# Kernel optimization log

Measured on AMD Instinct MI355X. Metric: run time of the kernel, lower is better.

Reference implementation:

```python
import jax, jax.numpy as jnp
import numpy as np

N = 50000       # nodes
E = 1600000     # edges (before self-loops)
DIN = 128       # input_dim
HID = 32        # hidden_dim per head
H = 4           # num_heads
HD = HID * H    # 128, concat-head width
DOUT = 128      # output_dim
NC = 2          # num_classes
G = 256         # graphs in batch
NEG_SLOPE = 0.2
BN_EPS = 1e-5


def setup_inputs() -> dict:
    key = jax.random.key(0)
    ks = jax.random.split(key, 20)
    p = lambda k, shp: (jax.random.normal(k, shp, jnp.float32) * 0.05)
    x = jax.random.normal(ks[0], (N, DIN), jnp.float32)
    edge_index = jax.random.randint(ks[1], (2, E), 0, N, dtype=jnp.int32)
    batch = jnp.sort(jax.random.randint(ks[2], (N,), 0, G, dtype=jnp.int32))
    return {
        "x": x, "edge_index": edge_index, "batch": batch,
        # GATConv 1: lin weight [DIN, H*HID], att vectors [H, HID], bias [H*HID]
        "W1": p(ks[3], (DIN, HD)), "a1_src": p(ks[4], (H, HID)), "a1_dst": p(ks[5], (H, HID)), "b1": p(ks[6], (HD,)),
        "bn1_g": jnp.ones((HD,), jnp.float32), "bn1_b": jnp.zeros((HD,), jnp.float32),
        # GATConv 2: in = H*HID
        "W2": p(ks[7], (HD, HD)), "a2_src": p(ks[8], (H, HID)), "a2_dst": p(ks[9], (H, HID)), "b2": p(ks[10], (HD,)),
        "bn2_g": jnp.ones((HD,), jnp.float32), "bn2_b": jnp.zeros((HD,), jnp.float32),
        "L1W": p(ks[11], (HD, DOUT)), "L1b": p(ks[12], (DOUT,)),
        "L2W": p(ks[13], (DOUT, NC)), "L2b": p(ks[14], (NC,)),
    }


def _add_self_loops(edge_index, n):
    loops = jnp.arange(n, dtype=edge_index.dtype)
    return jnp.concatenate([edge_index, jnp.stack([loops, loops])], axis=1)


def _gat_conv(x, edge_index, W, a_src, a_dst, bias):
    # PyG GATConv: h = x @ W -> [N,H,F]; per-edge score = LeakyReLU(a_src.h_src + a_dst.h_dst);
    # softmax over incoming edges of each dst node; weighted scatter-add; concat heads + bias.
    n = x.shape[0]
    h = (x @ W).reshape(n, H, HID)
    src, dst = edge_index[0], edge_index[1]
    alpha_s = jnp.sum(h * a_src[None], axis=-1)   # [N,H]
    alpha_d = jnp.sum(h * a_dst[None], axis=-1)   # [N,H]
    e = jax.nn.leaky_relu(alpha_s[src] + alpha_d[dst], NEG_SLOPE)  # [E,H]
    m = jax.ops.segment_max(e, dst, num_segments=n)                # stable softmax over neighbors
    ex = jnp.exp(e - m[dst])
    s = jax.ops.segment_sum(ex, dst, num_segments=n)
    alpha = ex / (s[dst] + 1e-16)                                  # [E,H]
    out = jax.ops.segment_sum(h[src] * alpha[:, :, None], dst, num_segments=n)  # [N,H,F]
    return out.reshape(n, H * HID) + bias


def _batch_norm(x, gamma, beta):
    mu = jnp.mean(x, axis=0)
    var = jnp.mean((x - mu) ** 2, axis=0)
    return gamma * (x - mu) * jax.lax.rsqrt(var + BN_EPS) + beta


def reference(x, edge_index, batch, W1, a1_src, a1_dst, b1, bn1_g, bn1_b,
              W2, a2_src, a2_dst, b2, bn2_g, bn2_b, L1W, L1b, L2W, L2b):
    ei = _add_self_loops(edge_index, x.shape[0])
    h = jax.nn.relu(_gat_conv(x, ei, W1, a1_src, a1_dst, b1))
    h = _batch_norm(h, bn1_g, bn1_b)
    h = jax.nn.relu(_gat_conv(h, ei, W2, a2_src, a2_dst, b2))
    h = _batch_norm(h, bn2_g, bn2_b)
    # global mean pool over graph ids
    sums = jax.ops.segment_sum(h, batch, num_segments=G)
    cnts = jax.ops.segment_sum(jnp.ones((h.shape[0],), h.dtype), batch, num_segments=G)
    pooled = sums / jnp.maximum(cnts, 1.0)[:, None]   # [G, HD]
    z = jax.nn.relu(pooled @ L1W + L1b)               # dropout inactive at eval
    return z @ L2W + L2b                              # [G, NC]
```

## Files before the change

### kernel.cpp

```cpp
#include <hip/hip_runtime.h>
#include <math.h>

#define NN 50000
#define EE 1600000
#define GG 256
#define PAD 80
#define NB 256
#define EPB 6250
#define NR 8
#define RNG 6250
#define BCAP 960
#define BNPB 512
#define BNPR 98

constexpr float NEG = 0.2f;
constexpr float BN_EPS = 1e-5f;

typedef __attribute__((ext_vector_type(8))) short short8;
typedef __attribute__((ext_vector_type(4))) float f32x4;
typedef __attribute__((ext_vector_type(2))) float f32x2;

constexpr int PB_W1 = 0, PB_A1S = 16384, PB_A1D = 16512, PB_B1 = 16640,
              PB_G1 = 16768, PB_BE1 = 16896, PB_W2 = 17024, PB_A2S = 33408,
              PB_A2D = 33536, PB_B2 = 33664, PB_G2 = 33792, PB_BE2 = 33920,
              PB_L1W = 34048, PB_L1B = 50432, PB_L2W = 50560, PB_L2B = 50816,
              PB_TOTAL = 50818;

struct PtrPack { const void* p[16]; };

__device__ __forceinline__ float b2f(unsigned short u) {
  unsigned v = ((unsigned)u) << 16;
  float f;
  __builtin_memcpy(&f, &v, 4);
  return f;
}
__device__ __forceinline__ float b2f_lo(unsigned u) {
  unsigned v = u << 16;
  float f;
  __builtin_memcpy(&f, &v, 4);
  return f;
}
__device__ __forceinline__ float b2f_hi(unsigned u) {
  unsigned v = u & 0xffff0000u;
  float f;
  __builtin_memcpy(&f, &v, 4);
  return f;
}
__device__ __forceinline__ unsigned short f2b(float f) {
  unsigned x;
  __builtin_memcpy(&x, &f, 4);
  unsigned r = x + 0x7FFFu + ((x >> 16) & 1u);
  return (unsigned short)(r >> 16);
}

__device__ __forceinline__ void pkfma(f32x2& acc, unsigned u, f32x2 wp) {
  f32x2 p = {b2f_lo(u), b2f_hi(u)};
  asm("v_pk_fma_f32 %0, %1, %2, %0" : "+v"(acc) : "v"(p), "v"(wp));
}

__global__ __launch_bounds__(512) void k_prep(PtrPack pk, const unsigned short* __restrict__ xb,
                                              const int* __restrict__ batch,
                                              const int* __restrict__ esrc,
                                              const int* __restrict__ edst,
                                              int* __restrict__ flag,
                                              float* __restrict__ pb,
                                              int* __restrict__ starts, float* __restrict__ bnacc,
                                              int* __restrict__ ctrs,
                                              unsigned char* __restrict__ hist,
                                              unsigned* __restrict__ buck, int* __restrict__ bcnt,
                                              unsigned short* __restrict__ Wt1,
                                              float* __restrict__ wzero,
                                              float* __restrict__ poolsum) {
  const int segoff[17] = {0, 16384, 16512, 16640, 16768, 16896, 17024, 33408,
                          33536, 33664, 33792, 33920, 34048, 50432, 50560, 50816, 50818};
  __shared__ unsigned hcnt[25000];
  __shared__ int bc[NR];
  __shared__ int cs;
  int c = blockIdx.x, t = threadIdx.x;
  if (t == 0) cs = 0;
  if (t < NR) bc[t] = 0;
  for (int j = t; j < 25000; j += 512) hcnt[j] = 0u;
  __syncthreads();
  int sane = 0;
  for (int i = t; i < 4096; i += 512) {
    float a = fabsf(b2f(xb[i]));
    if (a > 1e-4f && a < 100.f) sane++;
  }
  atomicAdd(&cs, sane);
  int e0 = c * EPB;
  for (int i = t; i < EPB; i += 512) {
    int e = e0 + i;
    int d = edst[e];
    if ((unsigned)d >= (unsigned)NN) continue;
    int s = esrc[e];
    if ((unsigned)s >= (unsigned)NN) s = 0;
    int sh = (d & 1) * 16;
    unsigned old = atomicAdd(&hcnt[d >> 1], 1u << sh);
    unsigned rank = (old >> sh) & 0xFFFFu;
    if (rank > 7u) continue;
    int r = d / RNG;
    int dl = d - r * RNG;
    int pos = atomicAdd(&bc[r], 1);
    if (pos < BCAP)
      buck[(c * NR + r) * BCAP + pos] = ((unsigned)s << 16) | ((unsigned)dl << 3) | rank;
  }
  __syncthreads();
  int bf = (cs > 3482) ? 1 : 0;
  if (c == 0 && t == 0) *flag = bf;
  if (t < NR) bcnt[c * NR + t] = min(bc[t], BCAP);
  unsigned* hw = (unsigned*)(hist + c * NN);
  for (int j = t; j < NN / 4; j += 512) {
    unsigned w0 = hcnt[2 * j], w1 = hcnt[2 * j + 1];
    unsigned b0 = min(w0 & 0xFFFFu, 255u), b1 = min(w0 >> 16, 255u);
    unsigned b2 = min(w1 & 0xFFFFu, 255u), b3 = min(w1 >> 16, 255u);
    hw[j] = b0 | (b1 << 8) | (b2 << 16) | (b3 << 24);
  }
  for (int j = t; j < 199; j += 512) {
    int i = c * 199 + j;
    if (i < PB_TOTAL) {
      int seg = 0;
      while (i >= segoff[seg + 1]) seg++;
      int k = i - segoff[seg];
      pb[i] = bf ? b2f(((const unsigned short*)pk.p[seg])[k]) : ((const float*)pk.p[seg])[k];
    }
  }
  for (int j = t; j < 64; j += 512) {
    int i = c * 64 + j;
    int n = i & 127, k = i >> 7;
    Wt1[n * 128 + k] = bf ? ((const unsigned short*)pk.p[0])[k * 128 + n]
                          : f2b(((const float*)pk.p[0])[k * 128 + n]);
  }
  for (int j = t; j < 128; j += 512) poolsum[c * 128 + j] = 0.f;
  if (t < 32) bnacc[c * 32 + t] = 0.f;
  for (int j = t; j < 196; j += 512) {
    int n = c * 196 + j;
    if (n < NN) {
      int bb = batch[n];
      bb = min(max(bb, 0), GG - 1);
      int bp = (n == 0) ? -1 : batch[n - 1];
      bp = min(max(bp, -1), GG - 1);
      for (int gg = bp + 1; gg <= bb; gg++) starts[gg] = n;
      if (n == NN - 1)
        for (int gg = bb + 1; gg <= GG; gg++) starts[gg] = NN;
    }
  }
  if (c == 255 && t < 8) ctrs[t] = 0;
}

__device__ __forceinline__ void gemm_body(float* cst, int bid,
                                          const unsigned short* __restrict__ Xb,
                                          const float* __restrict__ Xf, int bfm,
                                          const unsigned short* __restrict__ Wt,
                                          const float* __restrict__ shiftW,
                                          const float* __restrict__ aS,
                                          const float* __restrict__ aD,
                                          unsigned short* __restrict__ Y,
                                          float* __restrict__ as_, float* __restrict__ ad_) {
  int t = threadIdx.x;
  int row0 = bid * 64;
  int w = t >> 6, lane = t & 63;
  int m = lane & 15, quad = lane >> 4;
  int rA = min(row0 + w * 16 + m, NN - 1);
  short8 a4[4];
  if (bfm) {
    const short8* xp = (const short8*)(Xb + rA * 128);
#pragma unroll
    for (int kk = 0; kk < 4; kk++) a4[kk] = xp[kk * 4 + quad];
  } else {
#pragma unroll
    for (int kk = 0; kk < 4; kk++) {
      const float* xf = Xf + rA * 128 + kk * 32 + quad * 8;
#pragma unroll
      for (int j = 0; j < 8; j++) a4[kk][j] = (short)f2b(xf[j]);
    }
  }
  f32x4 acc[8] = {};
#pragma unroll
  for (int kk = 0; kk < 4; kk++) {
    int ko = kk * 32 + quad * 8;
#pragma unroll
    for (int n0 = 0; n0 < 8; n0++) {
      short8 b = *(const short8*)(Wt + (n0 * 16 + m) * 128 + ko);
      acc[n0] = __builtin_amdgcn_mfma_f32_16x16x32_bf16(a4[kk], b, acc[n0], 0, 0, 0);
    }
  }
#pragma unroll
  for (int n0 = 0; n0 < 8; n0++)
#pragma unroll
    for (int r = 0; r < 4; r++)
      cst[(w * 16 + quad * 4 + r) * 130 + n0 * 16 + m] = acc[n0][r];
  __syncthreads();
  int cg = t & 31, rg = t >> 5;
  int c0 = cg * 4;
  float a_s[4], a_d[4], sw[4];
#pragma unroll
  for (int j = 0; j < 4; j++) {
    a_s[j] = aS[c0 + j];
    a_d[j] = aD[c0 + j];
    sw[j] = shiftW[c0 + j];
  }
#pragma unroll
  for (int i = 0; i < 8; i++) {
    int rl = rg + i * 8;
    int row = row0 + rl;
    float v0 = cst[rl * 130 + c0 + 0] + sw[0];
    float v1 = cst[rl * 130 + c0 + 1] + sw[1];
    float v2 = cst[rl * 130 + c0 + 2] + sw[2];
    float v3 = cst[rl * 130 + c0 + 3] + sw[3];
    if (row < NN) {
      uint2 pk2;
      pk2.x = (unsigned)f2b(v0) | ((unsigned)f2b(v1) << 16);
      pk2.y = (unsigned)f2b(v2) | ((unsigned)f2b(v3) << 16);
      *reinterpret_cast<uint2*>(&Y[row * 128 + c0]) = pk2;
    }
    float ps = v0 * a_s[0] + v1 * a_s[1] + v2 * a_s[2] + v3 * a_s[3];
    float pd = v0 * a_d[0] + v1 * a_d[1] + v2 * a_d[2] + v3 * a_d[3];
    ps += __shfl_xor(ps, 1); ps += __shfl_xor(ps, 2); ps += __shfl_xor(ps, 4);
    pd += __shfl_xor(pd, 1); pd += __shfl_xor(pd, 2); pd += __shfl_xor(pd, 4);
    if ((cg & 7) == 0 && row < NN) {
      int hh = cg >> 3;
      as_[row * 4 + hh] = ps;
      ad_[row * 4 + hh] = pd;
    }
  }
}

__global__ __launch_bounds__(256) void k_basegemm(unsigned char* __restrict__ hist,
                                                  int* __restrict__ cnt,
                                                  const unsigned short* __restrict__ Xb,
                                                  const float* __restrict__ Xf,
                                                  const int* __restrict__ flagp,
                                                  const unsigned short* __restrict__ Wt,
                                                  const float* __restrict__ shiftW,
                                                  const float* __restrict__ aS,
                                                  const float* __restrict__ aD,
                                                  unsigned short* __restrict__ Y,
                                                  float* __restrict__ as_, float* __restrict__ ad_) {
  __shared__ float cst[64 * 130];
  int idx = blockIdx.x;
  if (idx < 196) {
    int d = idx * 256 + threadIdx.x;
    if (d >= NN) return;
    int run = 0;
    for (int b = 0; b < NB; b += 16) {
      unsigned char h[16];
#pragma unroll
      for (int j = 0; j < 16; j++) h[j] = hist[(b + j) * NN + d];
#pragma unroll
      for (int j = 0; j < 16; j++) {
        hist[(b + j) * NN + d] = (unsigned char)min(run, 255);
        run += h[j];
      }
    }
    cnt[d] = run;
  } else {
    gemm_body(cst, idx - 196, Xb, Xf, *flagp, Wt, shiftW, aS, aD, Y, as_, ad_);
  }
}

__global__ __launch_bounds__(256) void k_fill(const unsigned* __restrict__ buck,
                                              const int* __restrict__ bcnt,
                                              const unsigned char* __restrict__ base,
                                              unsigned short* __restrict__ adj) {
  int idx = blockIdx.x;
  int t = threadIdx.x;
  int r = idx & 7, g = idx >> 3;
  int dbase = r * RNG;
#pragma unroll 1
  for (int j = 0; j < 8; j++) {
    int c = g * 8 + j;
    int n = bcnt[c * NR + r];
    const unsigned* bk = buck + (c * NR + r) * BCAP;
    const unsigned char* bs = base + c * NN;
    for (int i = t; i < n; i += 256) {
      unsigned p = bk[i];
      int s = p >> 16;
      int dl = (p >> 3) & 0x1FFF;
      int rank = p & 7;
      int d = dbase + dl;
      int slot = (int)bs[d] + rank;
      if (slot < PAD) adj[d * PAD + slot] = (unsigned short)s;
    }
  }
}

__global__ __launch_bounds__(256) void k_gemm(const unsigned short* __restrict__ Xb,
                                              const unsigned short* __restrict__ Wt,
                                              const float* __restrict__ shiftW,
                                              const float* __restrict__ aS,
                                              const float* __restrict__ aD,
                                              unsigned short* __restrict__ Y,
                                              float* __restrict__ as_, float* __restrict__ ad_) {
  __shared__ float cst[64 * 130];
  gemm_body(cst, blockIdx.x, Xb, nullptr, 1, Wt, shiftW, aS, aD, Y, as_, ad_);
}

__global__ __launch_bounds__(256) void k_agg(const unsigned short* __restrict__ adj,
                                             const int* __restrict__ cnt,
                                             const float4* __restrict__ asrc4,
                                             const float4* __restrict__ adst4,
                                             const uint4* __restrict__ hin4,
                                             const float* __restrict__ bias,
                                             unsigned short* __restrict__ out) {
  __shared__ float wq2[4][4][PAD];
  __shared__ unsigned soffs[4][PAD];
  int t = threadIdx.x;
  int wid = t >> 6, lane = t & 63;
  int n = blockIdx.x * 4 + wid;
  int deg = cnt[n];
  if (deg < 0) deg = 0;
  if (deg > PAD - 1) deg = PAD - 1;
  int tot = deg + 1;
  int W = (((tot + 3) >> 2) + 3) & ~3;
  int WL = 4 * W;
  int beg = n * PAD;
  float4 ad4 = adst4[n];
  float ls0 = 0.f, ls1 = 0.f, ls2 = 0.f, ls3 = 0.f;
  for (int b = lane; b < WL; b += 64) {
    if (b < tot) {
      int s = (b < deg) ? (int)adj[beg + b] : n;
      if ((unsigned)s >= (unsigned)NN) s = n;
      float4 a = asrc4[s];
      float s0 = a.x + ad4.x; s0 = s0 > 0.f ? s0 : NEG * s0;
      float s1 = a.y + ad4.y; s1 = s1 > 0.f ? s1 : NEG * s1;
      float s2 = a.z + ad4.z; s2 = s2 > 0.f ? s2 : NEG * s2;
      float s3 = a.w + ad4.w; s3 = s3 > 0.f ? s3 : NEG * s3;
      float e0 = __expf(s0), e1 = __expf(s1), e2 = __expf(s2), e3 = __expf(s3);
      ls0 += e0; ls1 += e1; ls2 += e2; ls3 += e3;
      wq2[wid][0][b] = e0; wq2[wid][1][b] = e1;
      wq2[wid][2][b] = e2; wq2[wid][3][b] = e3;
      soffs[wid][b] = (unsigned)s * 256u;
    } else {
      wq2[wid][0][b] = 0.f; wq2[wid][1][b] = 0.f;
      wq2[wid][2][b] = 0.f; wq2[wid][3][b] = 0.f;
      soffs[wid][b] = (unsigned)n * 256u;
    }
  }
  asm volatile("" ::: "memory");
  __builtin_amdgcn_wave_barrier();
  int g = lane >> 4, L = lane & 15, hd = L >> 2;
  const char* hb = (const char*)hin4;
  unsigned Loff = (unsigned)L * 16u;
  const float* wrow = &wq2[wid][hd][0];
  const unsigned* srow = &soffs[wid][0];
  f32x2 acc2[4] = {};
  int e0w = g * W, e1w = e0w + W;
  for (int e = e0w; e < e1w; e += 4) {
    f32x4 w4 = *(const f32x4*)(wrow + e);
    uint4 o4 = *(const uint4*)(srow + e);
    uint4 v1 = *(const uint4*)(hb + (o4.x + Loff));
    uint4 v2 = *(const uint4*)(hb + (o4.y + Loff));
    uint4 v3 = *(const uint4*)(hb + (o4.z + Loff));
    uint4 v4 = *(const uint4*)(hb + (o4.w + Loff));
    f32x2 p1 = {w4.x, w4.x}, p2 = {w4.y, w4.y}, p3 = {w4.z, w4.z}, p4 = {w4.w, w4.w};
    pkfma(acc2[0], v1.x, p1); pkfma(acc2[1], v1.y, p1);
    pkfma(acc2[2], v1.z, p1); pkfma(acc2[3], v1.w, p1);
    pkfma(acc2[0], v2.x, p2); pkfma(acc2[1], v2.y, p2);
    pkfma(acc2[2], v2.z, p2); pkfma(acc2[3], v2.w, p2);
    pkfma(acc2[0], v3.x, p3); pkfma(acc2[1], v3.y, p3);
    pkfma(acc2[2], v3.z, p3); pkfma(acc2[3], v3.w, p3);
    pkfma(acc2[0], v4.x, p4); pkfma(acc2[1], v4.y, p4);
    pkfma(acc2[2], v4.z, p4); pkfma(acc2[3], v4.w, p4);
  }
#pragma unroll
  for (int j = 0; j < 4; j++) {
    acc2[j].x += __shfl_xor(acc2[j].x, 16);
    acc2[j].y += __shfl_xor(acc2[j].y, 16);
    acc2[j].x += __shfl_xor(acc2[j].x, 32);
    acc2[j].y += __shfl_xor(acc2[j].y, 32);
  }
#pragma unroll
  for (int mm = 1; mm < 64; mm <<= 1) {
    ls0 += __shfl_xor(ls0, mm);
    ls1 += __shfl_xor(ls1, mm);
    ls2 += __shfl_xor(ls2, mm);
    ls3 += __shfl_xor(ls3, mm);
  }
  if (g == 0) {
    float den = (hd == 0) ? ls0 : (hd == 1) ? ls1 : (hd == 2) ? ls2 : ls3;
    float inv = 1.0f / (den + 1e-16f);
    const float4* bp = reinterpret_cast<const float4*>(bias + L * 8);
    float4 b0 = bp[0], b1 = bp[1];
    float o0 = acc2[0].x * inv + b0.x;
    float o1 = acc2[0].y * inv + b0.y;
    float o2 = acc2[1].x * inv + b0.z;
    float o3 = acc2[1].y * inv + b0.w;
    float o4 = acc2[2].x * inv + b1.x;
    float o5 = acc2[2].y * inv + b1.y;
    float o6 = acc2[3].x * inv + b1.z;
    float o7 = acc2[3].y * inv + b1.w;
    o0 = o0 > 0.f ? o0 : 0.f;
    o1 = o1 > 0.f ? o1 : 0.f;
    o2 = o2 > 0.f ? o2 : 0.f;
    o3 = o3 > 0.f ? o3 : 0.f;
    o4 = o4 > 0.f ? o4 : 0.f;
    o5 = o5 > 0.f ? o5 : 0.f;
    o6 = o6 > 0.f ? o6 : 0.f;
    o7 = o7 > 0.f ? o7 : 0.f;
    uint4 pk4;
    pk4.x = (unsigned)f2b(o0) | ((unsigned)f2b(o1) << 16);
    pk4.y = (unsigned)f2b(o2) | ((unsigned)f2b(o3) << 16);
    pk4.z = (unsigned)f2b(o4) | ((unsigned)f2b(o5) << 16);
    pk4.w = (unsigned)f2b(o6) | ((unsigned)f2b(o7) << 16);
    *reinterpret_cast<uint4*>(&out[n * 128 + L * 8]) = pk4;
  }
}

__global__ __launch_bounds__(256) void k_bnpartial(const unsigned* __restrict__ x32,
                                                   float* __restrict__ partial,
                                                   const int* __restrict__ starts,
                                                   float* __restrict__ poolsum) {
  __shared__ float stg[4][256];
  int bid = blockIdx.x, t = threadIdx.x;
  int u = t & 63, ph = t >> 6;
  if (bid < BNPB) {
    int r0 = bid * BNPR, r1 = min(r0 + BNPR, NN);
    float s0 = 0.f, q0 = 0.f, s1 = 0.f, q1 = 0.f;
    for (int r = r0 + ph; r < r1; r += 4) {
      unsigned v = x32[r * 64 + u];
      float lo = b2f_lo(v), hi = b2f_hi(v);
      s0 += lo; q0 += lo * lo;
      s1 += hi; q1 += hi * hi;
    }
    stg[ph][2 * u] = s0;
    stg[ph][2 * u + 1] = s1;
    stg[ph][128 + 2 * u] = q0;
    stg[ph][128 + 2 * u + 1] = q1;
    __syncthreads();
    partial[bid * 256 + t] = stg[0][t] + stg[1][t] + stg[2][t] + stg[3][t];
  } else {
    int g = bid - BNPB;
    int b0 = starts[g], b1 = starts[g + 1];
    b0 = min(max(b0, 0), NN);
    b1 = min(max(b1, 0), NN);
    float p0 = 0.f, p1 = 0.f;
    for (int r = b0 + ph; r < b1; r += 4) {
      unsigned v = x32[r * 64 + u];
      p0 += b2f_lo(v);
      p1 += b2f_hi(v);
    }
    stg[ph][2 * u] = p0;
    stg[ph][2 * u + 1] = p1;
    __syncthreads();
    if (t < 128) poolsum[g * 128 + t] = stg[0][t] + stg[1][t] + stg[2][t] + stg[3][t];
  }
}

__global__ __launch_bounds__(256) void k_bnfinal(const float* __restrict__ partial,
                                                 const float* __restrict__ g, const float* __restrict__ b,
                                                 float* __restrict__ scale, float* __restrict__ shift,
                                                 const float* __restrict__ W2f, float* __restrict__ sw2,
                                                 unsigned short* __restrict__ Wt2) {
  __shared__ float sums[256];
  __shared__ float shs[128];
  __shared__ float scs[128];
  int t = threadIdx.x;
  float acc = 0.f;
  for (int bb = 0; bb < BNPB; bb += 8) {
    float a0 = partial[(bb + 0) * 256 + t];
    float a1 = partial[(bb + 1) * 256 + t];
    float a2 = partial[(bb + 2) * 256 + t];
    float a3 = partial[(bb + 3) * 256 + t];
    float a4 = partial[(bb + 4) * 256 + t];
    float a5 = partial[(bb + 5) * 256 + t];
    float a6 = partial[(bb + 6) * 256 + t];
    float a7 = partial[(bb + 7) * 256 + t];
    acc += ((a0 + a1) + (a2 + a3)) + ((a4 + a5) + (a6 + a7));
  }
  sums[t] = acc;
  __syncthreads();
  if (t < 128) {
    float inv = 1.0f / NN;
    float mu = sums[t] * inv;
    float var = sums[128 + t] * inv - mu * mu;
    float rs = rsqrtf(var + BN_EPS);
    float sc = g[t] * rs;
    float shv = b[t] - mu * sc;
    scale[t] = sc;
    shift[t] = shv;
    shs[t] = shv;
    scs[t] = sc;
  }
  __syncthreads();
  if (W2f) {
    if (t < 128) {
      float s = 0.f;
      for (int k = 0; k < 128; k++) s += shs[k] * W2f[k * 128 + t];
      sw2[t] = s;
    }
    for (int i = t; i < 16384; i += 256) {
      int n = i & 127, k = i >> 7;
      Wt2[n * 128 + k] = f2b(scs[k] * W2f[k * 128 + n]);
    }
  }
}

__global__ __launch_bounds__(128) void k_head(const float* __restrict__ poolsum,
                                              const int* __restrict__ starts,
                                              const float* __restrict__ scale, const float* __restrict__ shift,
                                              const float* __restrict__ L1W, const float* __restrict__ L1b,
                                              const float* __restrict__ L2W, const float* __restrict__ L2b,
                                              const int* __restrict__ flagp, void* __restrict__ outp) {
  int g = blockIdx.x, t = threadIdx.x;
  int b0 = starts[g], b1 = starts[g + 1];
  b0 = min(max(b0, 0), NN);
  b1 = min(max(b1, 0), NN);
  int cnt = b1 - b0;
  __shared__ float pooled[128];
  float s = poolsum[g * 128 + t];
  pooled[t] = (cnt > 0) ? (s / cnt) * scale[t] + shift[t] : 0.f;
  __syncthreads();
  float z = L1b[t];
  for (int k = 0; k < 128; k++) z += pooled[k] * L1W[k * 128 + t];
  z = z > 0.f ? z : 0.f;
  __shared__ float r0a[128], r1a[128];
  r0a[t] = z * L2W[t * 2 + 0];
  r1a[t] = z * L2W[t * 2 + 1];
  __syncthreads();
  for (int d = 64; d >= 1; d >>= 1) {
    if (t < d) {
      r0a[t] += r0a[t + d];
      r1a[t] += r1a[t + d];
    }
    __syncthreads();
  }
  if (t == 0) {
    float o0 = r0a[0] + L2b[0];
    float o1 = r1a[0] + L2b[1];
    if (*flagp) {
      unsigned short* ob = (unsigned short*)outp;
      ob[g * 2 + 0] = f2b(o0);
      ob[g * 2 + 1] = f2b(o1);
    } else {
      float* of = (float*)outp;
      of[g * 2 + 0] = o0;
      of[g * 2 + 1] = o1;
    }
  }
}

extern "C" void kernel_launch(void* const* d_in, const int* in_sizes, int n_in,
                              void* d_out, int out_size, void* d_ws, size_t ws_size,
                              hipStream_t stream) {
  (void)in_sizes; (void)n_in; (void)out_size; (void)ws_size;
  const int* ei = (const int*)d_in[1];
  const int* batch = (const int*)d_in[2];

  float* ws = (float*)d_ws;
  size_t o = 0;
  int* flag = (int*)(ws + o);   o += 16;
  int* ctrs = (int*)(ws + o);   o += 16;
  float* pb = ws + o;           o += 51200;
  float* bnacc = ws + o;        o += 8192;
  float* bnpart = ws + o;       o += BNPB * 256;
  float* scale1 = ws + o;       o += 128;
  float* shift1 = ws + o;       o += 128;
  float* scale2 = ws + o;       o += 128;
  float* shift2 = ws + o;       o += 128;
  float* wzero = ws + o;        o += 128;
  float* sw2 = ws + o;          o += 128;
  unsigned short* Wt1 = (unsigned short*)(ws + o); o += 8192;
  unsigned short* Wt2 = (unsigned short*)(ws + o); o += 8192;
  float* poolsum = ws + o;      o += GG * 128;
  int* cnt = (int*)(ws + o);    o += 50016;
  int* starts = (int*)(ws + o); o += 512;
  int* bcnt = (int*)(ws + o);   o += 2048;
  float* asrc = ws + o;         o += 200000;
  float* adst = ws + o;         o += 200000;
  unsigned* buck = (unsigned*)(ws + o);            o += NB * NR * BCAP;
  unsigned short* adj = (unsigned short*)(ws + o); o += NN * PAD / 2;
  unsigned short* hA = (unsigned short*)(ws + o);  o += 3200000;
  unsigned short* hB = (unsigned short*)(ws + o);  o += 3200000;

  unsigned char* hist = (unsigned char*)hA;

  const int* esrc = ei;
  const int* edst = ei + EE;

  PtrPack pk;
  for (int i = 0; i < 16; i++) pk.p[i] = d_in[3 + i];

  k_prep<<<NB, 512, 0, stream>>>(pk, (const unsigned short*)d_in[0], batch, esrc, edst,
                                 flag, pb, starts, bnacc, ctrs, hist, buck, bcnt,
                                 Wt1, wzero, poolsum);

  k_basegemm<<<196 + 782, 256, 0, stream>>>(hist, cnt,
                                            (const unsigned short*)d_in[0], (const float*)d_in[0],
                                            flag, Wt1, wzero,
                                            pb + PB_A1S, pb + PB_A1D, hB, asrc, adst);
  k_fill<<<NB, 256, 0, stream>>>(buck, bcnt, hist, adj);
  k_agg<<<NN / 4, 256, 0, stream>>>(adj, cnt, (const float4*)asrc, (const float4*)adst,
                                    (const uint4*)hB, pb + PB_B1, hA);
  k_bnpartial<<<BNPB, 256, 0, stream>>>((const unsigned*)hA, bnpart, starts, nullptr);
  k_bnfinal<<<1, 256, 0, stream>>>(bnpart, pb + PB_G1, pb + PB_BE1, scale1, shift1,
                                   pb + PB_W2, sw2, Wt2);

  k_gemm<<<782, 256, 0, stream>>>(hA, Wt2, sw2, pb + PB_A2S, pb + PB_A2D, hB, asrc, adst);
  k_agg<<<NN / 4, 256, 0, stream>>>(adj, cnt, (const float4*)asrc, (const float4*)adst,
                                    (const uint4*)hB, pb + PB_B2, hA);
  k_bnpartial<<<BNPB + GG, 256, 0, stream>>>((const unsigned*)hA, bnpart, starts, poolsum);
  k_bnfinal<<<1, 256, 0, stream>>>(bnpart, pb + PB_G2, pb + PB_BE2, scale2, shift2,
                                   nullptr, nullptr, nullptr);

  k_head<<<GG, 128, 0, stream>>>(poolsum, starts, scale2, shift2,
                                 pb + PB_L1W, pb + PB_L1B,
                                 pb + PB_L2W, pb + PB_L2B, flag, d_out);
}
```

Measured before the change: 358.6 us.

## Split prep kernel into edge and misc kernels; fold final BN stats into head

The monolithic prep kernel becomes two kernels. One does the edge bucketing and histogram with its large shared-memory table, and a lighter 256-thread kernel handles the format detection, parameter conversion and graph starts. The second single-block BN-final launch is removed: every head block now reduces the 512 BN partials itself and computes scale and shift before pooling. This removes a serial one-block launch, at the cost of 256 blocks redundantly reading the partial buffer. The intent is also that the misc prep work no longer has to run inside the low-occupancy shared-memory-heavy blocks.

```diff
diff --git a/kernel.cpp b/kernel.cpp
--- a/kernel.cpp
+++ b/kernel.cpp
@@ -58,35 +58,17 @@
   asm("v_pk_fma_f32 %0, %1, %2, %0" : "+v"(acc) : "v"(p), "v"(wp));
 }
 
-__global__ __launch_bounds__(512) void k_prep(PtrPack pk, const unsigned short* __restrict__ xb,
-                                              const int* __restrict__ batch,
-                                              const int* __restrict__ esrc,
-                                              const int* __restrict__ edst,
-                                              int* __restrict__ flag,
-                                              float* __restrict__ pb,
-                                              int* __restrict__ starts, float* __restrict__ bnacc,
-                                              int* __restrict__ ctrs,
-                                              unsigned char* __restrict__ hist,
-                                              unsigned* __restrict__ buck, int* __restrict__ bcnt,
-                                              unsigned short* __restrict__ Wt1,
-                                              float* __restrict__ wzero,
-                                              float* __restrict__ poolsum) {
-  const int segoff[17] = {0, 16384, 16512, 16640, 16768, 16896, 17024, 33408,
-                          33536, 33664, 33792, 33920, 34048, 50432, 50560, 50816, 50818};
+__global__ __launch_bounds__(512) void k_prep_edges(const int* __restrict__ esrc,
+                                                    const int* __restrict__ edst,
+                                                    unsigned char* __restrict__ hist,
+                                                    unsigned* __restrict__ buck,
+                                                    int* __restrict__ bcnt) {
   __shared__ unsigned hcnt[25000];
   __shared__ int bc[NR];
-  __shared__ int cs;
   int c = blockIdx.x, t = threadIdx.x;
-  if (t == 0) cs = 0;
   if (t < NR) bc[t] = 0;
   for (int j = t; j < 25000; j += 512) hcnt[j] = 0u;
   __syncthreads();
-  int sane = 0;
-  for (int i = t; i < 4096; i += 512) {
-    float a = fabsf(b2f(xb[i]));
-    if (a > 1e-4f && a < 100.f) sane++;
-  }
-  atomicAdd(&cs, sane);
   int e0 = c * EPB;
   for (int i = t; i < EPB; i += 512) {
     int e = e0 + i;
@@ -105,8 +87,6 @@
       buck[(c * NR + r) * BCAP + pos] = ((unsigned)s << 16) | ((unsigned)dl << 3) | rank;
   }
   __syncthreads();
-  int bf = (cs > 3482) ? 1 : 0;
-  if (c == 0 && t == 0) *flag = bf;
   if (t < NR) bcnt[c * NR + t] = min(bc[t], BCAP);
   unsigned* hw = (unsigned*)(hist + c * NN);
   for (int j = t; j < NN / 4; j += 512) {
@@ -115,7 +95,32 @@
     unsigned b2 = min(w1 & 0xFFFFu, 255u), b3 = min(w1 >> 16, 255u);
     hw[j] = b0 | (b1 << 8) | (b2 << 16) | (b3 << 24);
   }
-  for (int j = t; j < 199; j += 512) {
+}
+
+__global__ __launch_bounds__(256) void k_prep_misc(PtrPack pk, const unsigned short* __restrict__ xb,
+                                                   const int* __restrict__ batch,
+                                                   int* __restrict__ flag,
+                                                   float* __restrict__ pb,
+                                                   int* __restrict__ starts,
+                                                   int* __restrict__ ctrs,
+                                                   unsigned short* __restrict__ Wt1,
+                                                   float* __restrict__ poolsum) {
+  const int segoff[17] = {0, 16384, 16512, 16640, 16768, 16896, 17024, 33408,
+                          33536, 33664, 33792, 33920, 34048, 50432, 50560, 50816, 50818};
+  __shared__ int cs;
+  int c = blockIdx.x, t = threadIdx.x;
+  if (t == 0) cs = 0;
+  __syncthreads();
+  int sane = 0;
+  for (int i = t; i < 4096; i += 256) {
+    float a = fabsf(b2f(xb[i]));
+    if (a > 1e-4f && a < 100.f) sane++;
+  }
+  atomicAdd(&cs, sane);
+  __syncthreads();
+  int bf = (cs > 3482) ? 1 : 0;
+  if (c == 0 && t == 0) *flag = bf;
+  for (int j = t; j < 199; j += 256) {
     int i = c * 199 + j;
     if (i < PB_TOTAL) {
       int seg = 0;
@@ -124,15 +129,14 @@
       pb[i] = bf ? b2f(((const unsigned short*)pk.p[seg])[k]) : ((const float*)pk.p[seg])[k];
     }
   }
-  for (int j = t; j < 64; j += 512) {
+  for (int j = t; j < 64; j += 256) {
     int i = c * 64 + j;
     int n = i & 127, k = i >> 7;
     Wt1[n * 128 + k] = bf ? ((const unsigned short*)pk.p[0])[k * 128 + n]
                           : f2b(((const float*)pk.p[0])[k * 128 + n]);
   }
-  for (int j = t; j < 128; j += 512) poolsum[c * 128 + j] = 0.f;
-  if (t < 32) bnacc[c * 32 + t] = 0.f;
-  for (int j = t; j < 196; j += 512) {
+  for (int j = t; j < 128; j += 256) poolsum[c * 128 + j] = 0.f;
+  for (int j = t; j < 196; j += 256) {
     int n = c * 196 + j;
     if (n < NN) {
       int bb = batch[n];
@@ -448,7 +452,6 @@
 
 __global__ __launch_bounds__(256) void k_bnfinal(const float* __restrict__ partial,
                                                  const float* __restrict__ g, const float* __restrict__ b,
-                                                 float* __restrict__ scale, float* __restrict__ shift,
                                                  const float* __restrict__ W2f, float* __restrict__ sw2,
                                                  unsigned short* __restrict__ Wt2) {
   __shared__ float sums[256];
@@ -474,48 +477,72 @@
     float mu = sums[t] * inv;
     float var = sums[128 + t] * inv - mu * mu;
     float rs = rsqrtf(var + BN_EPS);
-    float sc = g[t] * rs;
-    float shv = b[t] - mu * sc;
-    scale[t] = sc;
-    shift[t] = shv;
-    shs[t] = shv;
-    scs[t] = sc;
-  }
-  __syncthreads();
-  if (W2f) {
-    if (t < 128) {
-      float s = 0.f;
-      for (int k = 0; k < 128; k++) s += shs[k] * W2f[k * 128 + t];
-      sw2[t] = s;
-    }
-    for (int i = t; i < 16384; i += 256) {
-      int n = i & 127, k = i >> 7;
-      Wt2[n * 128 + k] = f2b(scs[k] * W2f[k * 128 + n]);
-    }
-  }
-}
-
-__global__ __launch_bounds__(128) void k_head(const float* __restrict__ poolsum,
+    scs[t] = g[t] * rs;
+    shs[t] = b[t] - mu * scs[t];
+  }
+  __syncthreads();
+  if (t < 128) {
+    float s = 0.f;
+    for (int k = 0; k < 128; k++) s += shs[k] * W2f[k * 128 + t];
+    sw2[t] = s;
+  }
+  for (int i = t; i < 16384; i += 256) {
+    int n = i & 127, k = i >> 7;
+    Wt2[n * 128 + k] = f2b(scs[k] * W2f[k * 128 + n]);
+  }
+}
+
+__global__ __launch_bounds__(256) void k_head(const float* __restrict__ partial,
+                                              const float* __restrict__ poolsum,
                                               const int* __restrict__ starts,
-                                              const float* __restrict__ scale, const float* __restrict__ shift,
+                                              const float* __restrict__ g, const float* __restrict__ b,
                                               const float* __restrict__ L1W, const float* __restrict__ L1b,
                                               const float* __restrict__ L2W, const float* __restrict__ L2b,
                                               const int* __restrict__ flagp, void* __restrict__ outp) {
-  int g = blockIdx.x, t = threadIdx.x;
-  int b0 = starts[g], b1 = starts[g + 1];
+  __shared__ float sums[256];
+  __shared__ float scs[128], shs[128];
+  __shared__ float pooled[128];
+  __shared__ float r0a[128], r1a[128];
+  int gid = blockIdx.x, t = threadIdx.x;
+  float acc = 0.f;
+  for (int bb = 0; bb < BNPB; bb += 8) {
+    float a0 = partial[(bb + 0) * 256 + t];
+    float a1 = partial[(bb + 1) * 256 + t];
+    float a2 = partial[(bb + 2) * 256 + t];
+    float a3 = partial[(bb + 3) * 256 + t];
+    float a4 = partial[(bb + 4) * 256 + t];
+    float a5 = partial[(bb + 5) * 256 + t];
+    float a6 = partial[(bb + 6) * 256 + t];
+    float a7 = partial[(bb + 7) * 256 + t];
+    acc += ((a0 + a1) + (a2 + a3)) + ((a4 + a5) + (a6 + a7));
+  }
+  sums[t] = acc;
+  __syncthreads();
+  if (t < 128) {
+    float inv = 1.0f / NN;
+    float mu = sums[t] * inv;
+    float var = sums[128 + t] * inv - mu * mu;
+    float rs = rsqrtf(var + BN_EPS);
+    scs[t] = g[t] * rs;
+    shs[t] = b[t] - mu * scs[t];
+  }
+  __syncthreads();
+  int b0 = starts[gid], b1 = starts[gid + 1];
   b0 = min(max(b0, 0), NN);
   b1 = min(max(b1, 0), NN);
   int cnt = b1 - b0;
-  __shared__ float pooled[128];
-  float s = poolsum[g * 128 + t];
-  pooled[t] = (cnt > 0) ? (s / cnt) * scale[t] + shift[t] : 0.f;
-  __syncthreads();
-  float z = L1b[t];
-  for (int k = 0; k < 128; k++) z += pooled[k] * L1W[k * 128 + t];
-  z = z > 0.f ? z : 0.f;
-  __shared__ float r0a[128], r1a[128];
-  r0a[t] = z * L2W[t * 2 + 0];
-  r1a[t] = z * L2W[t * 2 + 1];
+  if (t < 128) {
+    float s = poolsum[gid * 128 + t];
+    pooled[t] = (cnt > 0) ? (s / cnt) * scs[t] + shs[t] : 0.f;
+  }
+  __syncthreads();
+  if (t < 128) {
+    float z = L1b[t];
+    for (int k = 0; k < 128; k++) z += pooled[k] * L1W[k * 128 + t];
+    z = z > 0.f ? z : 0.f;
+    r0a[t] = z * L2W[t * 2 + 0];
+    r1a[t] = z * L2W[t * 2 + 1];
+  }
   __syncthreads();
   for (int d = 64; d >= 1; d >>= 1) {
     if (t < d) {
@@ -529,12 +556,12 @@
     float o1 = r1a[0] + L2b[1];
     if (*flagp) {
       unsigned short* ob = (unsigned short*)outp;
-      ob[g * 2 + 0] = f2b(o0);
-      ob[g * 2 + 1] = f2b(o1);
+      ob[gid * 2 + 0] = f2b(o0);
+      ob[gid * 2 + 1] = f2b(o1);
     } else {
       float* of = (float*)outp;
-      of[g * 2 + 0] = o0;
-      of[g * 2 + 1] = o1;
+      of[gid * 2 + 0] = o0;
+      of[gid * 2 + 1] = o1;
     }
   }
 }
@@ -551,12 +578,7 @@
   int* flag = (int*)(ws + o);   o += 16;
   int* ctrs = (int*)(ws + o);   o += 16;
   float* pb = ws + o;           o += 51200;
-  float* bnacc = ws + o;        o += 8192;
   float* bnpart = ws + o;       o += BNPB * 256;
-  float* scale1 = ws + o;       o += 128;
-  float* shift1 = ws + o;       o += 128;
-  float* scale2 = ws + o;       o += 128;
-  float* shift2 = ws + o;       o += 128;
   float* wzero = ws + o;        o += 128;
   float* sw2 = ws + o;          o += 128;
   unsigned short* Wt1 = (unsigned short*)(ws + o); o += 8192;
@@ -580,9 +602,9 @@
   PtrPack pk;
   for (int i = 0; i < 16; i++) pk.p[i] = d_in[3 + i];
 
-  k_prep<<<NB, 512, 0, stream>>>(pk, (const unsigned short*)d_in[0], batch, esrc, edst,
-                                 flag, pb, starts, bnacc, ctrs, hist, buck, bcnt,
-                                 Wt1, wzero, poolsum);
+  k_prep_edges<<<NB, 512, 0, stream>>>(esrc, edst, hist, buck, bcnt);
+  k_prep_misc<<<256, 256, 0, stream>>>(pk, (const unsigned short*)d_in[0], batch,
+                                       flag, pb, starts, ctrs, Wt1, poolsum);
 
   k_basegemm<<<196 + 782, 256, 0, stream>>>(hist, cnt,
                                             (const unsigned short*)d_in[0], (const float*)d_in[0],
@@ -592,17 +614,16 @@
   k_agg<<<NN / 4, 256, 0, stream>>>(adj, cnt, (const float4*)asrc, (const float4*)adst,
                                     (const uint4*)hB, pb + PB_B1, hA);
   k_bnpartial<<<BNPB, 256, 0, stream>>>((const unsigned*)hA, bnpart, starts, nullptr);
-  k_bnfinal<<<1, 256, 0, stream>>>(bnpart, pb + PB_G1, pb + PB_BE1, scale1, shift1,
+  k_bnfinal<<<1, 256, 0, stream>>>(bnpart, pb + PB_G1, pb + PB_BE1,
                                    pb + PB_W2, sw2, Wt2);
 
   k_gemm<<<782, 256, 0, stream>>>(hA, Wt2, sw2, pb + PB_A2S, pb + PB_A2D, hB, asrc, adst);
   k_agg<<<NN / 4, 256, 0, stream>>>(adj, cnt, (const float4*)asrc, (const float4*)adst,
                                     (const uint4*)hB, pb + PB_B2, hA);
   k_bnpartial<<<BNPB + GG, 256, 0, stream>>>((const unsigned*)hA, bnpart, starts, poolsum);
-  k_bnfinal<<<1, 256, 0, stream>>>(bnpart, pb + PB_G2, pb + PB_BE2, scale2, shift2,
-                                   nullptr, nullptr, nullptr);
-
-  k_head<<<GG, 128, 0, stream>>>(poolsum, starts, scale2, shift2,
+
+  k_head<<<GG, 256, 0, stream>>>(bnpart, poolsum, starts,
+                                 pb + PB_G2, pb + PB_BE2,
                                  pb + PB_L1W, pb + PB_L1B,
                                  pb + PB_L2W, pb + PB_L2B, flag, d_out);
 }
```

Result: no change. 357.4 us (-0.3%).
